# Kernel optimization log

Measured on AMD Instinct MI355X. Metric: run time of the kernel, lower is better.

Reference implementation:

```python
import jax, jax.numpy as jnp
import numpy as np

B, N, D_IN = 256, 64, 128   # batch, n_agents, input_dim
H0, H1, H2 = 256, 256, 64   # rnn_hidden_dim[0], [1], [2]


def setup_inputs() -> dict:
    key = jax.random.key(0)
    ks = jax.random.split(key, 14)
    s = 0.05
    return {
        "obs": jax.random.normal(ks[0], (B, N, D_IN), dtype=jnp.float32),
        "W_enc": jax.random.normal(ks[1], (H0, D_IN), dtype=jnp.float32) * s,
        "b_enc": jax.random.normal(ks[2], (H0,), dtype=jnp.float32) * s,
        "W_obs": jax.random.normal(ks[3], (H0, H0), dtype=jnp.float32) * s,
        "b_obs": jax.random.normal(ks[4], (H0,), dtype=jnp.float32) * s,
        "W_ih": jax.random.normal(ks[5], (3 * H0, H0), dtype=jnp.float32) * s,
        "b_ih": jax.random.normal(ks[6], (3 * H0,), dtype=jnp.float32) * s,
        "W_hh": jax.random.normal(ks[7], (3 * H0, H0), dtype=jnp.float32) * s,
        "b_hh": jax.random.normal(ks[8], (3 * H0,), dtype=jnp.float32) * s,
        "W_val": jax.random.normal(ks[9], (H1, H0), dtype=jnp.float32) * s,
        "b_val": jax.random.normal(ks[10], (H1,), dtype=jnp.float32) * s,
        "W_dec": jax.random.normal(ks[11], (H2, H1), dtype=jnp.float32) * s,
        "b_dec": jax.random.normal(ks[12], (H2,), dtype=jnp.float32) * s,
    }


def reference(obs, W_enc, b_enc, W_obs, b_obs, W_ih, b_ih, W_hh, b_hh,
              W_val, b_val, W_dec, b_dec):
    # encoding + f_obs  -> h: [B, N, H0]
    x = jax.nn.relu(jnp.einsum("bnd,hd->bnh", obs, W_enc) + b_enc)
    h = jnp.einsum("bnh,gh->bng", x, W_obs) + b_obs

    # comm: mean over other agents. Original masks self and divides by N
    # (mean over dim of size N with self zeroed) => (sum_all - self) / N.
    c = (jnp.sum(h, axis=1, keepdims=True) - h) / N  # [B, N, H0]

    # GRUCell(input=c, hidden=h), PyTorch gate ordering r, z, n
    gi = jnp.einsum("bnh,gh->bng", c, W_ih) + b_ih   # [B, N, 3*H0]
    gh = jnp.einsum("bnh,gh->bng", h, W_hh) + b_hh
    gi_r, gi_z, gi_n = jnp.split(gi, 3, axis=-1)
    gh_r, gh_z, gh_n = jnp.split(gh, 3, axis=-1)
    r = jax.nn.sigmoid(gi_r + gh_r)
    z = jax.nn.sigmoid(gi_z + gh_z)
    n = jnp.tanh(gi_n + r * gh_n)
    h = (1.0 - z) * n + z * h  # [B, N, H0]

    # value head + decoding; seq_len=1 squeezed -> [B, N, H2]
    v = jnp.einsum("bnh,vh->bnv", h, W_val) + b_val
    out = jnp.einsum("bnv,ov->bno", v, W_dec) + b_dec
    return out
```

## Files before the change

### kernel.cpp

```cpp
#include <hip/hip_runtime.h>
#include <hip/hip_bf16.h>
#include <math.h>


typedef __bf16  bf16x8 __attribute__((ext_vector_type(8)));
typedef float   f32x4  __attribute__((ext_vector_type(4)));

#define DIN 128
#define H0  256
#define SW  264
#define SWO 136
#define LOG2E 1.44269504088896f

#define O_WENC 0
#define O_WOBS 32768
#define O_WIH  98304
#define O_WHH  294912
#define O_WVAL 491520
#define O_WDEC 557056
#define W_TOT  573440

__device__ __forceinline__ f32x4 mfma16(bf16x8 a, bf16x8 b, f32x4 c) {
    return __builtin_amdgcn_mfma_f32_16x16x32_bf16(a, b, c, 0, 0, 0);
}
__device__ __forceinline__ float bf2f(__hip_bfloat16 x) { return __bfloat162float(x); }
__device__ __forceinline__ __hip_bfloat16 f2bf(float x) { return __float2bfloat16(x); }

__device__ __forceinline__ float fsigmoid(float x) {
    float e = __builtin_amdgcn_exp2f(-LOG2E * x);
    return __builtin_amdgcn_rcpf(1.0f + e);
}
__device__ __forceinline__ float ftanh(float x) {
    float e = __builtin_amdgcn_exp2f(2.0f * LOG2E * x);
    return 1.0f - 2.0f * __builtin_amdgcn_rcpf(1.0f + e);
}

__device__ __forceinline__ bf16x8 w8(const __hip_bfloat16* p, int idx) {
    return *(const bf16x8*)(p + idx);
}

__device__ __forceinline__ int tadr(int r, int k) { return r * SW + k; }
__device__ __forceinline__ int oadr(int r, int k) { return r * SWO + k; }

__global__ __launch_bounds__(256) void prep_kernel(
    const float* __restrict__ W_enc, const float* __restrict__ W_obs,
    const float* __restrict__ W_ih,  const float* __restrict__ W_hh,
    const float* __restrict__ W_val, const float* __restrict__ W_dec,
    __hip_bfloat16* __restrict__ ws)
{
    const int i = (blockIdx.x * 256 + threadIdx.x) * 8;
    if (i >= W_TOT) return;
    const float* src; int off;
    if      (i < O_WOBS) { src = W_enc; off = O_WENC; }
    else if (i < O_WIH)  { src = W_obs; off = O_WOBS; }
    else if (i < O_WHH)  { src = W_ih;  off = O_WIH;  }
    else if (i < O_WVAL) { src = W_hh;  off = O_WHH;  }
    else if (i < O_WDEC) { src = W_val; off = O_WVAL; }
    else                 { src = W_dec; off = O_WDEC; }
    const float* f = src + (i - off);
    f32x4 a = *(const f32x4*)f;
    f32x4 b = *(const f32x4*)(f + 4);
    bf16x8 v;
    #pragma unroll
    for (int j = 0; j < 4; j++) { v[j] = (__bf16)a[j]; v[j + 4] = (__bf16)b[j]; }
    *(bf16x8*)(ws + i) = v;
}

__global__ __launch_bounds__(512, 2) void commnet_mfma(
    const __hip_bfloat16* __restrict__ ws,
    const float* __restrict__ b_enc, const float* __restrict__ b_obs,
    const float* __restrict__ b_ih,  const float* __restrict__ b_hh,
    const float* __restrict__ b_val, const float* __restrict__ b_dec,
    const float* __restrict__ obs,   float* __restrict__ out)
{
    __shared__ __align__(16) __hip_bfloat16 T0[64 * SW];
    __shared__ __align__(16) __hip_bfloat16 T1[64 * SW];

    const __hip_bfloat16* W_enc = ws + O_WENC;
    const __hip_bfloat16* W_obs = ws + O_WOBS;
    const __hip_bfloat16* W_ih  = ws + O_WIH;
    const __hip_bfloat16* W_hh  = ws + O_WHH;
    const __hip_bfloat16* W_val = ws + O_WVAL;
    const __hip_bfloat16* W_dec = ws + O_WDEC;

    const int tid  = threadIdx.x;
    const int wave = tid >> 6;
    const int lane = tid & 63;
    const int quad = lane >> 4;
    const int lc   = lane & 15;
    const int row0 = blockIdx.x * 64;
    const int ko16 = quad * 8;

    for (int i = tid; i < 64 * DIN / 8; i += 512) {
        const int r = i >> 4;
        const int c = (i & 15) << 3;
        const float* src = obs + (row0 + r) * DIN + c;
        f32x4 a = *(const f32x4*)src;
        f32x4 b = *(const f32x4*)(src + 4);
        bf16x8 v;
        #pragma unroll
        for (int j = 0; j < 4; j++) { v[j] = (__bf16)a[j]; v[j + 4] = (__bf16)b[j]; }
        *(bf16x8*)&T1[oadr(r, c)] = v;
    }
    __syncthreads();

    #pragma unroll
    for (int cp = 0; cp < 2; cp++) {
        const int n = (wave + 8 * cp) * 16 + lc;
        const float bias = b_enc[n];
        f32x4 acc[4] = {};
        #pragma unroll
        for (int k0 = 0; k0 < DIN; k0 += 32) {
            const int kk = k0 + ko16;
            bf16x8 b = w8(W_enc, n * DIN + kk);
            #pragma unroll
            for (int rt = 0; rt < 4; rt++) {
                bf16x8 a = *(const bf16x8*)&T1[oadr(rt * 16 + lc, kk)];
                acc[rt] = mfma16(a, b, acc[rt]);
            }
        }
        #pragma unroll
        for (int rt = 0; rt < 4; rt++)
            #pragma unroll
            for (int i = 0; i < 4; i++) {
                const int row = rt * 16 + quad * 4 + i;
                T0[tadr(row, n)] = f2bf(fmaxf(acc[rt][i] + bias, 0.0f));
            }
    }
    __syncthreads();

    #pragma unroll
    for (int cp = 0; cp < 2; cp++) {
        const int n = (wave + 8 * cp) * 16 + lc;
        const float bias = b_obs[n];
        f32x4 acc[4] = {};
        #pragma unroll
        for (int k0 = 0; k0 < H0; k0 += 32) {
            const int kk = k0 + ko16;
            bf16x8 b = w8(W_obs, n * H0 + kk);
            #pragma unroll
            for (int rt = 0; rt < 4; rt++) {
                bf16x8 a = *(const bf16x8*)&T0[tadr(rt * 16 + lc, kk)];
                acc[rt] = mfma16(a, b, acc[rt]);
            }
        }
        #pragma unroll
        for (int rt = 0; rt < 4; rt++)
            #pragma unroll
            for (int i = 0; i < 4; i++) {
                const int row = rt * 16 + quad * 4 + i;
                T1[tadr(row, n)] = f2bf(acc[rt][i] + bias);
            }
    }
    __syncthreads();

    #pragma unroll
    for (int cp = 0; cp < 2; cp++) {
        const int n = (wave + 8 * cp) * 16 + lc;
        const float bir = b_ih[n], biz = b_ih[n + 256], bin = b_ih[n + 512];
        const float bhr = b_hh[n], bhz = b_hh[n + 256], bhn = b_hh[n + 512];
        f32x4 gir[4] = {}, giz[4] = {}, gin[4] = {};
        f32x4 ghr[4] = {}, ghz[4] = {}, ghn[4] = {};
        #pragma unroll 4
        for (int k0 = 0; k0 < H0; k0 += 32) {
            const int kk = k0 + ko16;
            bf16x8 bir8 = w8(W_ih, (n      ) * H0 + kk);
            bf16x8 biz8 = w8(W_ih, (n + 256) * H0 + kk);
            bf16x8 bin8 = w8(W_ih, (n + 512) * H0 + kk);
            bf16x8 bhr8 = w8(W_hh, (n      ) * H0 + kk);
            bf16x8 bhz8 = w8(W_hh, (n + 256) * H0 + kk);
            bf16x8 bhn8 = w8(W_hh, (n + 512) * H0 + kk);
            #pragma unroll
            for (int rt = 0; rt < 4; rt++) {
                bf16x8 aH = *(const bf16x8*)&T1[tadr(rt * 16 + lc, kk)];
                gir[rt] = mfma16(aH, bir8, gir[rt]);
                giz[rt] = mfma16(aH, biz8, giz[rt]);
                gin[rt] = mfma16(aH, bin8, gin[rt]);
                ghr[rt] = mfma16(aH, bhr8, ghr[rt]);
                ghz[rt] = mfma16(aH, bhz8, ghz[rt]);
                ghn[rt] = mfma16(aH, bhn8, ghn[rt]);
            }
        }
        float Sr = 0.0f, Sz = 0.0f, Sn = 0.0f;
        #pragma unroll
        for (int rt = 0; rt < 4; rt++)
            #pragma unroll
            for (int i = 0; i < 4; i++) {
                Sr += gir[rt][i]; Sz += giz[rt][i]; Sn += gin[rt][i];
            }
        Sr += __shfl_xor(Sr, 16); Sr += __shfl_xor(Sr, 32);
        Sz += __shfl_xor(Sz, 16); Sz += __shfl_xor(Sz, 32);
        Sn += __shfl_xor(Sn, 16); Sn += __shfl_xor(Sn, 32);

        #pragma unroll
        for (int rt = 0; rt < 4; rt++)
            #pragma unroll
            for (int i = 0; i < 4; i++) {
                const int row = rt * 16 + quad * 4 + i;
                const float gi_r = (Sr - gir[rt][i]) * (1.0f / 64.0f) + bir;
                const float gi_z = (Sz - giz[rt][i]) * (1.0f / 64.0f) + biz;
                const float gi_n = (Sn - gin[rt][i]) * (1.0f / 64.0f) + bin;
                const float r  = fsigmoid(gi_r + ghr[rt][i] + bhr);
                const float z  = fsigmoid(gi_z + ghz[rt][i] + bhz);
                const float nn = ftanh(gi_n + r * (ghn[rt][i] + bhn));
                const float h  = bf2f(T1[tadr(row, n)]);
                T0[tadr(row, n)] = f2bf((1.0f - z) * nn + z * h);
            }
    }
    __syncthreads();

    #pragma unroll
    for (int cp = 0; cp < 2; cp++) {
        const int n = (wave + 8 * cp) * 16 + lc;
        const float bias = b_val[n];
        f32x4 acc[4] = {};
        #pragma unroll
        for (int k0 = 0; k0 < H0; k0 += 32) {
            const int kk = k0 + ko16;
            bf16x8 b = w8(W_val, n * H0 + kk);
            #pragma unroll
            for (int rt = 0; rt < 4; rt++) {
                bf16x8 a = *(const bf16x8*)&T0[tadr(rt * 16 + lc, kk)];
                acc[rt] = mfma16(a, b, acc[rt]);
            }
        }
        #pragma unroll
        for (int rt = 0; rt < 4; rt++)
            #pragma unroll
            for (int i = 0; i < 4; i++) {
                const int row = rt * 16 + quad * 4 + i;
                T1[tadr(row, n)] = f2bf(acc[rt][i] + bias);
            }
    }
    __syncthreads();

    {
        const int ct  = wave & 3;
        const int rtb = (wave >> 2) * 2;
        const int n   = ct * 16 + lc;
        const float bias = b_dec[n];
        f32x4 acc[2] = {};
        #pragma unroll
        for (int k0 = 0; k0 < H0; k0 += 32) {
            const int kk = k0 + ko16;
            bf16x8 b = w8(W_dec, n * H0 + kk);
            #pragma unroll
            for (int j = 0; j < 2; j++) {
                bf16x8 a = *(const bf16x8*)&T1[tadr((rtb + j) * 16 + lc, kk)];
                acc[j] = mfma16(a, b, acc[j]);
            }
        }
        #pragma unroll
        for (int j = 0; j < 2; j++)
            #pragma unroll
            for (int i = 0; i < 4; i++) {
                const int row = (rtb + j) * 16 + quad * 4 + i;
                out[(row0 + row) * 64 + n] = acc[j][i] + bias;
            }
    }
}

extern "C" void kernel_launch(void* const* d_in, const int* in_sizes, int n_in,
                              void* d_out, int out_size, void* d_ws, size_t ws_size,
                              hipStream_t stream) {
    (void)in_sizes; (void)n_in; (void)out_size; (void)ws_size;
    const float* obs   = (const float*)d_in[0];
    const float* W_enc = (const float*)d_in[1];  const float* b_enc = (const float*)d_in[2];
    const float* W_obs = (const float*)d_in[3];  const float* b_obs = (const float*)d_in[4];
    const float* W_ih  = (const float*)d_in[5];  const float* b_ih  = (const float*)d_in[6];
    const float* W_hh  = (const float*)d_in[7];  const float* b_hh  = (const float*)d_in[8];
    const float* W_val = (const float*)d_in[9];  const float* b_val = (const float*)d_in[10];
    const float* W_dec = (const float*)d_in[11]; const float* b_dec = (const float*)d_in[12];
    float* out = (float*)d_out;
    __hip_bfloat16* ws = (__hip_bfloat16*)d_ws;

    prep_kernel<<<280, 256, 0, stream>>>(W_enc, W_obs, W_ih, W_hh, W_val, W_dec, ws);
    commnet_mfma<<<256, 512, 0, stream>>>(
        ws, b_enc, b_obs, b_ih, b_hh, b_val, b_dec, obs, out);
}
```

Before: 120.3 us.

## Use 1024-thread blocks so each wave owns one 16-column tile

The fused CommNet kernel now launches 1024 threads (16 waves) per 64-row block instead of 512, so each wave handles a single 16-column slice per layer instead of looping over two. The obs load becomes one vector per thread, and the decoder stage assigns one 16x16 output tile per wave. This aims to expose more parallelism per block and shorten each wave's serial MFMA chain. In exchange it raises per-block register pressure under launch_bounds(1024), limits residency to one large block per CU, and makes each block wait on more waves at every __syncthreads.

```diff
diff --git a/kernel.cpp b/kernel.cpp
--- a/kernel.cpp
+++ b/kernel.cpp
@@ -66,7 +66,7 @@
     *(bf16x8*)(ws + i) = v;
 }
 
-__global__ __launch_bounds__(512, 2) void commnet_mfma(
+__global__ __launch_bounds__(1024) void commnet_mfma(
     const __hip_bfloat16* __restrict__ ws,
     const float* __restrict__ b_enc, const float* __restrict__ b_obs,
     const float* __restrict__ b_ih,  const float* __restrict__ b_hh,
@@ -90,8 +90,10 @@
     const int lc   = lane & 15;
     const int row0 = blockIdx.x * 64;
     const int ko16 = quad * 8;
-
-    for (int i = tid; i < 64 * DIN / 8; i += 512) {
+    const int n    = wave * 16 + lc;
+
+    {
+        const int i = tid;
         const int r = i >> 4;
         const int c = (i & 15) << 3;
         const float* src = obs + (row0 + r) * DIN + c;
@@ -104,9 +106,7 @@
     }
     __syncthreads();
 
-    #pragma unroll
-    for (int cp = 0; cp < 2; cp++) {
-        const int n = (wave + 8 * cp) * 16 + lc;
+    {
         const float bias = b_enc[n];
         f32x4 acc[4] = {};
         #pragma unroll
@@ -129,9 +129,7 @@
     }
     __syncthreads();
 
-    #pragma unroll
-    for (int cp = 0; cp < 2; cp++) {
-        const int n = (wave + 8 * cp) * 16 + lc;
+    {
         const float bias = b_obs[n];
         f32x4 acc[4] = {};
         #pragma unroll
@@ -154,9 +152,7 @@
     }
     __syncthreads();
 
-    #pragma unroll
-    for (int cp = 0; cp < 2; cp++) {
-        const int n = (wave + 8 * cp) * 16 + lc;
+    {
         const float bir = b_ih[n], biz = b_ih[n + 256], bin = b_ih[n + 512];
         const float bhr = b_hh[n], bhz = b_hh[n + 256], bhn = b_hh[n + 512];
         f32x4 gir[4] = {}, giz[4] = {}, gin[4] = {};
@@ -209,9 +205,7 @@
     }
     __syncthreads();
 
-    #pragma unroll
-    for (int cp = 0; cp < 2; cp++) {
-        const int n = (wave + 8 * cp) * 16 + lc;
+    {
         const float bias = b_val[n];
         f32x4 acc[4] = {};
         #pragma unroll
@@ -235,28 +229,23 @@
     __syncthreads();
 
     {
-        const int ct  = wave & 3;
-        const int rtb = (wave >> 2) * 2;
-        const int n   = ct * 16 + lc;
-        const float bias = b_dec[n];
-        f32x4 acc[2] = {};
-        #pragma unroll
-        for (int k0 = 0; k0 < H0; k0 += 32) {
-            const int kk = k0 + ko16;
-            bf16x8 b = w8(W_dec, n * H0 + kk);
-            #pragma unroll
-            for (int j = 0; j < 2; j++) {
-                bf16x8 a = *(const bf16x8*)&T1[tadr((rtb + j) * 16 + lc, kk)];
-                acc[j] = mfma16(a, b, acc[j]);
-            }
-        }
-        #pragma unroll
-        for (int j = 0; j < 2; j++)
-            #pragma unroll
-            for (int i = 0; i < 4; i++) {
-                const int row = (rtb + j) * 16 + quad * 4 + i;
-                out[(row0 + row) * 64 + n] = acc[j][i] + bias;
-            }
+        const int ct = wave & 3;
+        const int rt = wave >> 2;
+        const int nd = ct * 16 + lc;
+        const float bias = b_dec[nd];
+        f32x4 acc = {};
+        #pragma unroll
+        for (int k0 = 0; k0 < H0; k0 += 32) {
+            const int kk = k0 + ko16;
+            bf16x8 b = w8(W_dec, nd * H0 + kk);
+            bf16x8 a = *(const bf16x8*)&T1[tadr(rt * 16 + lc, kk)];
+            acc = mfma16(a, b, acc);
+        }
+        #pragma unroll
+        for (int i = 0; i < 4; i++) {
+            const int row = rt * 16 + quad * 4 + i;
+            out[(row0 + row) * 64 + nd] = acc[i] + bias;
+        }
     }
 }
 
@@ -275,6 +264,6 @@
     __hip_bfloat16* ws = (__hip_bfloat16*)d_ws;
 
     prep_kernel<<<280, 256, 0, stream>>>(W_enc, W_obs, W_ih, W_hh, W_val, W_dec, ws);
-    commnet_mfma<<<256, 512, 0, stream>>>(
+    commnet_mfma<<<256, 1024, 0, stream>>>(
         ws, b_enc, b_obs, b_ih, b_hh, b_val, b_dec, obs, out);
 }
```

After: 183.6 us. 1.53x slower.
